# Performance work log

Hardware: AMD Instinct MI355X
Metric: run time of the kernel (lower is better)

Reference implementation:

```python
import jax, jax.numpy as jnp
import numpy as np

B, T, C = 2, 2048, 2048
NH, NKV = 32, 8
HD = C // NH          # 64
G = NH // NKV         # queries per kv head

def setup_inputs() -> dict:
    key = jax.random.key(0)
    ks = jax.random.split(key, 6)
    s = 0.02
    return {
        "x":  jax.random.normal(ks[0], (B, T, C), jnp.float32),
        "wq": jax.random.normal(ks[1], (C, C), jnp.float32) * s,
        "wk": jax.random.normal(ks[2], (C, NKV * HD), jnp.float32) * s,
        "wv": jax.random.normal(ks[3], (C, NKV * HD), jnp.float32) * s,
        "wp": jax.random.normal(ks[4], (C, C), jnp.float32) * s,
        "bp": jax.random.normal(ks[5], (C,), jnp.float32) * s,
    }

def reference(x, wq, wk, wv, wp, bp):
    Bb, Tt, Cc = x.shape
    # projections
    q = (x @ wq).reshape(Bb, Tt, NH, HD).transpose(0, 2, 1, 3)    # (B, NH, T, D)
    k = (x @ wk).reshape(Bb, Tt, NKV, HD).transpose(0, 2, 1, 3)   # (B, NKV, T, D)
    v = (x @ wv).reshape(Bb, Tt, NKV, HD).transpose(0, 2, 1, 3)
    # GQA: group query heads per kv head (equivalent to repeat_interleave on kv)
    qg = q.reshape(Bb, NKV, G, Tt, HD)                            # (B, NKV, G, T, D)
    att = jnp.einsum('bhgqd,bhkd->bhgqk', qg, k) * (HD ** -0.5)   # (B, NKV, G, T, T)
    causal = jnp.tril(jnp.ones((Tt, Tt), bool))
    att = jnp.where(causal, att, -jnp.inf)
    att = jax.nn.softmax(att, axis=-1)
    y = jnp.einsum('bhgqk,bhkd->bhgqd', att, v)                   # (B, NKV, G, T, D)
    y = y.reshape(Bb, NH, Tt, HD).transpose(0, 2, 1, 3).reshape(Bb, Tt, Cc)
    return y @ wp + bp
```

## Files before the change

kernel.cpp:

```cpp
#include <hip/hip_runtime.h>
#include <math.h>

#define B_   2
#define T_   2048
#define C_   2048
#define NH_  32
#define NKV_ 8
#define HD_  64
#define G_   (NH_ / NKV_)
#define M_   (B_ * T_)
#define C3_  3072

typedef __attribute__((ext_vector_type(8))) short  short8;
typedef __attribute__((ext_vector_type(4))) float  f32x4;

__device__ __forceinline__ short f2bf(float f) {
    unsigned u = __float_as_uint(f);
    unsigned r = (u + 0x7FFFu + ((u >> 16) & 1u)) >> 16;
    return (short)r;
}

__device__ __forceinline__ void gload_lds16(const void* g, void* l) {
    __builtin_amdgcn_global_load_lds(
        (const __attribute__((address_space(1))) unsigned int*)g,
        (__attribute__((address_space(3))) unsigned int*)l, 16, 0, 0);
}

__global__ __launch_bounds__(256)
void cast_f32_bf16(const float* __restrict__ in, short* __restrict__ out, int n8)
{
    int i = blockIdx.x * blockDim.x + threadIdx.x;
    const int stride = gridDim.x * blockDim.x;
    for (; i < n8; i += stride) {
        const float4 a = ((const float4*)in)[i * 2];
        const float4 b = ((const float4*)in)[i * 2 + 1];
        short8 v;
        v[0] = f2bf(a.x); v[1] = f2bf(a.y); v[2] = f2bf(a.z); v[3] = f2bf(a.w);
        v[4] = f2bf(b.x); v[5] = f2bf(b.y); v[6] = f2bf(b.z); v[7] = f2bf(b.w);
        ((short8*)out)[i] = v;
    }
}

__global__ __launch_bounds__(256)
void transpose_cast(const float* __restrict__ W, short* __restrict__ Wt,
                    int Nw, int rowOff)
{
    __shared__ float tileF[64][65];
    const int tid = threadIdx.x;
    const int n0 = blockIdx.x * 64;
    const int k0 = blockIdx.y * 64;

    #pragma unroll
    for (int it = 0; it < 4; ++it) {
        const int s = it * 256 + tid;
        const int r = s >> 4;
        const int c4 = (s & 15) * 4;
        const float4 v = *(const float4*)(W + (size_t)(k0 + r) * Nw + n0 + c4);
        tileF[r][c4 + 0] = v.x;
        tileF[r][c4 + 1] = v.y;
        tileF[r][c4 + 2] = v.z;
        tileF[r][c4 + 3] = v.w;
    }
    __syncthreads();
    #pragma unroll
    for (int it = 0; it < 2; ++it) {
        const int s = it * 256 + tid;
        const int n = s >> 3;
        const int kc = (s & 7) * 8;
        short8 v;
        #pragma unroll
        for (int j = 0; j < 8; ++j) v[j] = f2bf(tileF[kc + j][n]);
        *(short8*)&Wt[(size_t)(rowOff + n0 + n) * 2048 + k0 + kc] = v;
    }
}

__global__ __launch_bounds__(256)
void transpose_v_bf16(const short* __restrict__ QKVb, short* __restrict__ Vt)
{
    __shared__ short Ls[64 * 66];
    const int tid = threadIdx.x;
    const int t0  = blockIdx.x * 64;
    const int b   = blockIdx.y >> 3;
    const int kvh = blockIdx.y & 7;

    #pragma unroll
    for (int it = 0; it < 2; ++it) {
        const int s = it * 256 + tid;
        const int tr = s >> 3;
        const int c8 = (s & 7) * 8;
        const short8 v = *(const short8*)(
            QKVb + (size_t)(b * T_ + t0 + tr) * C3_ + 2560 + kvh * HD_ + c8);
        #pragma unroll
        for (int e = 0; e < 8; ++e) Ls[tr * 66 + c8 + e] = v[e];
    }
    __syncthreads();
    #pragma unroll
    for (int it = 0; it < 2; ++it) {
        const int s = it * 256 + tid;
        const int d  = s >> 3;
        const int t8 = (s & 7) * 8;
        short8 v;
        #pragma unroll
        for (int j = 0; j < 8; ++j) v[j] = Ls[(t8 + j) * 66 + d];
        *(short8*)(Vt + (size_t)(blockIdx.y * HD_ + d) * T_ + t0 + t8) = v;
    }
}

__global__ __launch_bounds__(256)
void gemm_bf16_bt(const short* __restrict__ A, const short* __restrict__ Bt,
                  float* __restrict__ C, short* __restrict__ Cb,
                  const float* __restrict__ bias, int M, int N, int K)
{
    __shared__ __attribute__((aligned(16))) short Als[128 * 32];
    __shared__ __attribute__((aligned(16))) short Bls[128 * 32];

    const int tid  = threadIdx.x;
    const int wave = tid >> 6;
    const int lane = tid & 63;

    const int gx   = gridDim.x;
    const int nwg  = gx * gridDim.y;
    const int orig = blockIdx.y * gx + blockIdx.x;
    const int qc   = nwg >> 3;
    const int rc   = nwg & 7;
    const int xcd  = orig & 7;
    const int wgid = (xcd < rc ? xcd * (qc + 1) : rc * (qc + 1) + (xcd - rc) * qc)
                     + (orig >> 3);
    const int m0 = (wgid / gx) * 128;
    const int n0 = (wgid % gx) * 128;

    const int wr = wave >> 1;
    const int wc = wave & 1;

    const int sr = lane >> 2;
    const int kq = (lane & 3) * 8;
    const int fr = lane & 15;
    const int fg = (lane >> 4) * 8;

    const short* Abase = A  + (size_t)m0 * K;
    const short* Bbase = Bt + (size_t)n0 * K;

    f32x4 acc[4][4];
    const f32x4 zero = {0.f, 0.f, 0.f, 0.f};
    #pragma unroll
    for (int i = 0; i < 4; ++i)
        #pragma unroll
        for (int j = 0; j < 4; ++j) acc[i][j] = zero;

    for (int k0 = 0; k0 < K; k0 += 32) {
        __syncthreads();
        #pragma unroll
        for (int i = 0; i < 2; ++i) {
            const int c = wave * 2 + i;
            const int row = c * 16 + sr;
            gload_lds16(Abase + (size_t)row * K + k0 + kq, &Als[c * 512]);
            gload_lds16(Bbase + (size_t)row * K + k0 + kq, &Bls[c * 512]);
        }
        __syncthreads();

        short8 af[4], bf[4];
        #pragma unroll
        for (int mi = 0; mi < 4; ++mi)
            af[mi] = *(const short8*)&Als[(wr * 64 + mi * 16 + fr) * 32 + fg];
        #pragma unroll
        for (int ni = 0; ni < 4; ++ni)
            bf[ni] = *(const short8*)&Bls[(wc * 64 + ni * 16 + fr) * 32 + fg];
        #pragma unroll
        for (int mi = 0; mi < 4; ++mi)
            #pragma unroll
            for (int ni = 0; ni < 4; ++ni)
                acc[mi][ni] = __builtin_amdgcn_mfma_f32_16x16x32_bf16(
                    af[mi], bf[ni], acc[mi][ni], 0, 0, 0);
    }

    const int rsub = (lane >> 4) * 4;
    const int ccol0 = n0 + wc * 64 + fr;
    #pragma unroll
    for (int mi = 0; mi < 4; ++mi) {
        const int mrow = m0 + wr * 64 + mi * 16 + rsub;
        #pragma unroll
        for (int ni = 0; ni < 4; ++ni) {
            const int col = ccol0 + ni * 16;
            const float badd = bias ? bias[col] : 0.f;
            #pragma unroll
            for (int r = 0; r < 4; ++r) {
                const float v = acc[mi][ni][r] + badd;
                if (Cb) Cb[(size_t)(mrow + r) * N + col] = f2bf(v);
                else    C [(size_t)(mrow + r) * N + col] = v;
            }
        }
    }
}

__global__ __launch_bounds__(256)
void attn_mfma(const short* __restrict__ QKVb, const short* __restrict__ Vt,
               short* __restrict__ Yb)
{
    __shared__ __attribute__((aligned(16))) short Kls[2][4096];
    __shared__ __attribute__((aligned(16))) short Vls[2][4096];
    __shared__ __attribute__((aligned(16))) short Pls[4096];

    const int tid  = threadIdx.x;
    const int wave = tid >> 6;
    const int lane = tid & 63;
    const int bh = blockIdx.y;
    const int b   = bh >> 5;
    const int h   = bh & 31;
    const int kvh = h >> 2;
    const int bx  = gridDim.x - 1 - blockIdx.x;
    const int m0 = bx * 64;
    const int qbase = m0 + wave * 16;

    const int fr = lane & 15;
    const int fg = (lane >> 4) * 8;
    const int g4 = (lane >> 4) * 4;

    const short* qrow = QKVb + (size_t)(b * T_ + qbase + fr) * C3_ + h * HD_;
    const short8 qa0 = *(const short8*)(qrow + fg);
    const short8 qa1 = *(const short8*)(qrow + 32 + fg);

    f32x4 accO[4];
    const f32x4 zero = {0.f, 0.f, 0.f, 0.f};
    #pragma unroll
    for (int i = 0; i < 4; ++i) accO[i] = zero;
    float lsum[4] = {0.f, 0.f, 0.f, 0.f};

    const int sr  = lane >> 3;
    const int scb = (lane & 7) * 16;
    const int ssw = (scb ^ ((sr & 7) << 4)) >> 1;
    const short* Kg = QKVb + (size_t)b * T_ * C3_ + 2048 + kvh * HD_ + ssw;
    const short* Vg = Vt + (size_t)(b * NKV_ + kvh) * HD_ * T_ + ssw;

    short* PlsW = Pls + wave * 1024;
    const char* PlsB = (const char*)PlsW;

    const int ntiles = bx + 1;
    const int frsw = (fr & 7) << 4;

    auto STAGE = [&](int t, int bsel) {
        const int ks = t * 64;
        #pragma unroll
        for (int i = 0; i < 2; ++i) {
            const int c = wave * 2 + i;
            gload_lds16(Kg + (size_t)(ks + c * 8 + sr) * C3_, &Kls[bsel][c * 512]);
            gload_lds16(Vg + (size_t)(c * 8 + sr) * T_ + ks,  &Vls[bsel][c * 512]);
        }
    };

    STAGE(0, 0);
    __syncthreads();

    int cur = 0;
    for (int t = 0; t < ntiles; ++t) {
        if (t + 1 < ntiles) STAGE(t + 1, cur ^ 1);

        const int ks = t * 64;
        const char* KlsB = (const char*)&Kls[cur][0];
        const char* VlsB = (const char*)&Vls[cur][0];

        f32x4 accS[4];
        #pragma unroll
        for (int jt = 0; jt < 4; ++jt) accS[jt] = zero;
        __builtin_amdgcn_s_setprio(1);
        #pragma unroll
        for (int jt = 0; jt < 4; ++jt) {
            const int row = jt * 16 + fr;
            const char* base = KlsB + row * 128;
            const short8 kb0 = *(const short8*)(base + ((fg * 2) ^ frsw));
            const short8 kb1 = *(const short8*)(base + (((32 + fg) * 2) ^ frsw));
            accS[jt] = __builtin_amdgcn_mfma_f32_16x16x32_bf16(qa0, kb0, accS[jt], 0, 0, 0);
            accS[jt] = __builtin_amdgcn_mfma_f32_16x16x32_bf16(qa1, kb1, accS[jt], 0, 0, 0);
        }
        __builtin_amdgcn_s_setprio(0);

        const bool full = (ks + 63 <= qbase);
        float pv[4][4];
        #pragma unroll
        for (int jt = 0; jt < 4; ++jt) {
            #pragma unroll
            for (int r = 0; r < 4; ++r) {
                const int j = ks + jt * 16 + fr;
                const int q = qbase + g4 + r;
                float p = __expf(fmaf(accS[jt][r], 0.125f, -4.0f));
                if (!full && j > q) p = 0.f;
                pv[jt][r] = p;
            }
        }
        #pragma unroll
        for (int r = 0; r < 4; ++r)
            lsum[r] += (pv[0][r] + pv[1][r]) + (pv[2][r] + pv[3][r]);

        #pragma unroll
        for (int jt = 0; jt < 4; ++jt) {
            #pragma unroll
            for (int r = 0; r < 4; ++r) {
                const int prow = g4 + r;
                const int pj = jt * 16 + fr;
                *(short*)((char*)PlsW + prow * 128 + ((pj * 2) ^ ((prow & 7) << 4)))
                    = f2bf(pv[jt][r]);
            }
        }

        __builtin_amdgcn_s_setprio(1);
        #pragma unroll
        for (int kk = 0; kk < 2; ++kk) {
            const int kcb = (kk * 32 + fg) * 2;
            const short8 pa = *(const short8*)(PlsB + fr * 128 + (kcb ^ frsw));
            #pragma unroll
            for (int ni = 0; ni < 4; ++ni) {
                const int row = ni * 16 + fr;
                const short8 vb = *(const short8*)(VlsB + row * 128 + (kcb ^ frsw));
                accO[ni] = __builtin_amdgcn_mfma_f32_16x16x32_bf16(pa, vb, accO[ni], 0, 0, 0);
            }
        }
        __builtin_amdgcn_s_setprio(0);

        if (t + 1 < ntiles) { __syncthreads(); cur ^= 1; }
    }

    #pragma unroll
    for (int r = 0; r < 4; ++r) {
        float v = lsum[r];
        v += __shfl_xor(v, 1);
        v += __shfl_xor(v, 2);
        v += __shfl_xor(v, 4);
        v += __shfl_xor(v, 8);
        lsum[r] = 1.f / v;
    }

    #pragma unroll
    for (int ni = 0; ni < 4; ++ni)
        #pragma unroll
        for (int r = 0; r < 4; ++r)
            PlsW[(g4 + r) * 64 + ni * 16 + fr] = f2bf(accO[ni][r] * lsum[r]);

    #pragma unroll
    for (int i = 0; i < 2; ++i) {
        const int lin = i * 1024 + lane * 16;
        const int rr = lin >> 7;
        const int cb = lin & 127;
        const short8 v = *(const short8*)(PlsB + lin);
        *(short8*)((char*)Yb + ((size_t)(b * T_ + qbase + rr) * C_ + h * HD_) * 2 + cb) = v;
    }
}

extern "C" void kernel_launch(void* const* d_in, const int* in_sizes, int n_in,
                              void* d_out, int out_size, void* d_ws, size_t ws_size,
                              hipStream_t stream)
{
    const float* x  = (const float*)d_in[0];
    const float* wq = (const float*)d_in[1];
    const float* wk = (const float*)d_in[2];
    const float* wv = (const float*)d_in[3];
    const float* wp = (const float*)d_in[4];
    const float* bp = (const float*)d_in[5];
    float* out = (float*)d_out;

    char* w = (char*)d_ws;
    short* xb   = (short*)w;
    short* wt   = (short*)(w + 16777216);
    short* QKVb = (short*)(w + 29360128);
    short* Vt   = (short*)(w + 54525952);
    short* Yb   = xb;
    short* wpt  = wt;

    const dim3 blk(256);

    cast_f32_bf16<<<2048, blk, 0, stream>>>(x, xb, M_ * C_ / 8);

    transpose_cast<<<dim3(32, 32), blk, 0, stream>>>(wq, wt, 2048, 0);
    transpose_cast<<<dim3(8, 32),  blk, 0, stream>>>(wk, wt, 512, 2048);
    transpose_cast<<<dim3(8, 32),  blk, 0, stream>>>(wv, wt, 512, 2560);

    gemm_bf16_bt<<<dim3(C3_ / 128, M_ / 128), blk, 0, stream>>>(
        xb, wt, nullptr, QKVb, nullptr, M_, C3_, C_);

    transpose_cast<<<dim3(32, 32), blk, 0, stream>>>(wp, wpt, 2048, 0);
    transpose_v_bf16<<<dim3(32, 16), blk, 0, stream>>>(QKVb, Vt);

    attn_mfma<<<dim3(T_ / 64, B_ * NH_), blk, 0, stream>>>(QKVb, Vt, Yb);

    gemm_bf16_bt<<<dim3(C_ / 128, M_ / 128), blk, 0, stream>>>(
        Yb, wpt, out, nullptr, bp, M_, C_, C_);
}
```

Measured before the change: 377.0 us.

## Process 128 query rows per attention block, two 16-row groups per wave

The attention kernel now gives each block 128 query rows, and each wave handles two 16-row groups that share the K/V tiles staged in LDS. Each staged K/V tile is reused across twice as many queries, which halves global and LDS staging traffic per query and the number of barriers per unit of work. Waves whose rows lie entirely before a tile skip its compute. The cost is higher register pressure, half as many blocks in the grid, and intra-block causal imbalance.

```diff
diff --git a/kernel.cpp b/kernel.cpp
--- a/kernel.cpp
+++ b/kernel.cpp
@@ -208,22 +208,27 @@
     const int h   = bh & 31;
     const int kvh = h >> 2;
     const int bx  = gridDim.x - 1 - blockIdx.x;
-    const int m0 = bx * 64;
-    const int qbase = m0 + wave * 16;
+    const int m0 = bx * 128;
+    const int qbase = m0 + wave * 32;
 
     const int fr = lane & 15;
     const int fg = (lane >> 4) * 8;
     const int g4 = (lane >> 4) * 4;
 
-    const short* qrow = QKVb + (size_t)(b * T_ + qbase + fr) * C3_ + h * HD_;
-    const short8 qa0 = *(const short8*)(qrow + fg);
-    const short8 qa1 = *(const short8*)(qrow + 32 + fg);
-
-    f32x4 accO[4];
+    const short* qrow0 = QKVb + (size_t)(b * T_ + qbase + fr) * C3_ + h * HD_;
+    const short* qrow1 = qrow0 + 16 * C3_;
+    const short8 qa00 = *(const short8*)(qrow0 + fg);
+    const short8 qa01 = *(const short8*)(qrow0 + 32 + fg);
+    const short8 qa10 = *(const short8*)(qrow1 + fg);
+    const short8 qa11 = *(const short8*)(qrow1 + 32 + fg);
+
+    f32x4 accO[2][4];
     const f32x4 zero = {0.f, 0.f, 0.f, 0.f};
     #pragma unroll
-    for (int i = 0; i < 4; ++i) accO[i] = zero;
-    float lsum[4] = {0.f, 0.f, 0.f, 0.f};
+    for (int rg = 0; rg < 2; ++rg)
+        #pragma unroll
+        for (int i = 0; i < 4; ++i) accO[rg][i] = zero;
+    float lsum[2][4] = {{0.f,0.f,0.f,0.f},{0.f,0.f,0.f,0.f}};
 
     const int sr  = lane >> 3;
     const int scb = (lane & 7) * 16;
@@ -234,7 +239,7 @@
     short* PlsW = Pls + wave * 1024;
     const char* PlsB = (const char*)PlsW;
 
-    const int ntiles = bx + 1;
+    const int ntiles = 2 * bx + 2;
     const int frsw = (fr & 7) << 4;
 
     auto STAGE = [&](int t, int bsel) {
@@ -258,89 +263,106 @@
         const char* KlsB = (const char*)&Kls[cur][0];
         const char* VlsB = (const char*)&Vls[cur][0];
 
-        f32x4 accS[4];
-        #pragma unroll
-        for (int jt = 0; jt < 4; ++jt) accS[jt] = zero;
-        __builtin_amdgcn_s_setprio(1);
-        #pragma unroll
-        for (int jt = 0; jt < 4; ++jt) {
-            const int row = jt * 16 + fr;
-            const char* base = KlsB + row * 128;
-            const short8 kb0 = *(const short8*)(base + ((fg * 2) ^ frsw));
-            const short8 kb1 = *(const short8*)(base + (((32 + fg) * 2) ^ frsw));
-            accS[jt] = __builtin_amdgcn_mfma_f32_16x16x32_bf16(qa0, kb0, accS[jt], 0, 0, 0);
-            accS[jt] = __builtin_amdgcn_mfma_f32_16x16x32_bf16(qa1, kb1, accS[jt], 0, 0, 0);
-        }
-        __builtin_amdgcn_s_setprio(0);
-
-        const bool full = (ks + 63 <= qbase);
-        float pv[4][4];
-        #pragma unroll
-        for (int jt = 0; jt < 4; ++jt) {
-            #pragma unroll
-            for (int r = 0; r < 4; ++r) {
-                const int j = ks + jt * 16 + fr;
-                const int q = qbase + g4 + r;
-                float p = __expf(fmaf(accS[jt][r], 0.125f, -4.0f));
-                if (!full && j > q) p = 0.f;
-                pv[jt][r] = p;
+        if (ks <= qbase + 31) {
+            f32x4 accS[2][4];
+            #pragma unroll
+            for (int rg = 0; rg < 2; ++rg)
+                #pragma unroll
+                for (int jt = 0; jt < 4; ++jt) accS[rg][jt] = zero;
+            __builtin_amdgcn_s_setprio(1);
+            #pragma unroll
+            for (int jt = 0; jt < 4; ++jt) {
+                const int row = jt * 16 + fr;
+                const char* base = KlsB + row * 128;
+                const short8 kb0 = *(const short8*)(base + ((fg * 2) ^ frsw));
+                const short8 kb1 = *(const short8*)(base + (((32 + fg) * 2) ^ frsw));
+                accS[0][jt] = __builtin_amdgcn_mfma_f32_16x16x32_bf16(qa00, kb0, accS[0][jt], 0, 0, 0);
+                accS[0][jt] = __builtin_amdgcn_mfma_f32_16x16x32_bf16(qa01, kb1, accS[0][jt], 0, 0, 0);
+                accS[1][jt] = __builtin_amdgcn_mfma_f32_16x16x32_bf16(qa10, kb0, accS[1][jt], 0, 0, 0);
+                accS[1][jt] = __builtin_amdgcn_mfma_f32_16x16x32_bf16(qa11, kb1, accS[1][jt], 0, 0, 0);
             }
-        }
-        #pragma unroll
-        for (int r = 0; r < 4; ++r)
-            lsum[r] += (pv[0][r] + pv[1][r]) + (pv[2][r] + pv[3][r]);
-
-        #pragma unroll
-        for (int jt = 0; jt < 4; ++jt) {
-            #pragma unroll
-            for (int r = 0; r < 4; ++r) {
-                const int prow = g4 + r;
-                const int pj = jt * 16 + fr;
-                *(short*)((char*)PlsW + prow * 128 + ((pj * 2) ^ ((prow & 7) << 4)))
-                    = f2bf(pv[jt][r]);
+            __builtin_amdgcn_s_setprio(0);
+
+            #pragma unroll
+            for (int rg = 0; rg < 2; ++rg) {
+                const int qb = qbase + rg * 16;
+                const bool full = (ks + 63 <= qb);
+
+                float pv[4][4];
+                #pragma unroll
+                for (int jt = 0; jt < 4; ++jt) {
+                    #pragma unroll
+                    for (int r = 0; r < 4; ++r) {
+                        const int j = ks + jt * 16 + fr;
+                        const int q = qb + g4 + r;
+                        float p = __expf(fmaf(accS[rg][jt][r], 0.125f, -4.0f));
+                        if (!full && j > q) p = 0.f;
+                        pv[jt][r] = p;
+                    }
+                }
+                #pragma unroll
+                for (int r = 0; r < 4; ++r)
+                    lsum[rg][r] += (pv[0][r] + pv[1][r]) + (pv[2][r] + pv[3][r]);
+
+                #pragma unroll
+                for (int jt = 0; jt < 4; ++jt) {
+                    #pragma unroll
+                    for (int r = 0; r < 4; ++r) {
+                        const int prow = g4 + r;
+                        const int pj = jt * 16 + fr;
+                        *(short*)((char*)PlsW + prow * 128 + ((pj * 2) ^ ((prow & 7) << 4)))
+                            = f2bf(pv[jt][r]);
+                    }
+                }
+
+                __builtin_amdgcn_s_setprio(1);
+                #pragma unroll
+                for (int kk = 0; kk < 2; ++kk) {
+                    const int kcb = (kk * 32 + fg) * 2;
+                    const short8 pa = *(const short8*)(PlsB + fr * 128 + (kcb ^ frsw));
+                    #pragma unroll
+                    for (int ni = 0; ni < 4; ++ni) {
+                        const int row = ni * 16 + fr;
+                        const short8 vb = *(const short8*)(VlsB + row * 128 + (kcb ^ frsw));
+                        accO[rg][ni] = __builtin_amdgcn_mfma_f32_16x16x32_bf16(pa, vb, accO[rg][ni], 0, 0, 0);
+                    }
+                }
+                __builtin_amdgcn_s_setprio(0);
             }
         }
 
-        __builtin_amdgcn_s_setprio(1);
-        #pragma unroll
-        for (int kk = 0; kk < 2; ++kk) {
-            const int kcb = (kk * 32 + fg) * 2;
-            const short8 pa = *(const short8*)(PlsB + fr * 128 + (kcb ^ frsw));
-            #pragma unroll
-            for (int ni = 0; ni < 4; ++ni) {
-                const int row = ni * 16 + fr;
-                const short8 vb = *(const short8*)(VlsB + row * 128 + (kcb ^ frsw));
-                accO[ni] = __builtin_amdgcn_mfma_f32_16x16x32_bf16(pa, vb, accO[ni], 0, 0, 0);
-            }
-        }
-        __builtin_amdgcn_s_setprio(0);
-
         if (t + 1 < ntiles) { __syncthreads(); cur ^= 1; }
     }
 
     #pragma unroll
-    for (int r = 0; r < 4; ++r) {
-        float v = lsum[r];
-        v += __shfl_xor(v, 1);
-        v += __shfl_xor(v, 2);
-        v += __shfl_xor(v, 4);
-        v += __shfl_xor(v, 8);
-        lsum[r] = 1.f / v;
-    }
-
-    #pragma unroll
-    for (int ni = 0; ni < 4; ++ni)
-        #pragma unroll
-        for (int r = 0; r < 4; ++r)
-            PlsW[(g4 + r) * 64 + ni * 16 + fr] = f2bf(accO[ni][r] * lsum[r]);
-
-    #pragma unroll
-    for (int i = 0; i < 2; ++i) {
-        const int lin = i * 1024 + lane * 16;
-        const int rr = lin >> 7;
-        const int cb = lin & 127;
-        const short8 v = *(const short8*)(PlsB + lin);
-        *(short8*)((char*)Yb + ((size_t)(b * T_ + qbase + rr) * C_ + h * HD_) * 2 + cb) = v;
+    for (int rg = 0; rg < 2; ++rg)
+        #pragma unroll
+        for (int r = 0; r < 4; ++r) {
+            float v = lsum[rg][r];
+            v += __shfl_xor(v, 1);
+            v += __shfl_xor(v, 2);
+            v += __shfl_xor(v, 4);
+            v += __shfl_xor(v, 8);
+            lsum[rg][r] = 1.f / v;
+        }
+
+    #pragma unroll
+    for (int rg = 0; rg < 2; ++rg) {
+        #pragma unroll
+        for (int ni = 0; ni < 4; ++ni)
+            #pragma unroll
+            for (int r = 0; r < 4; ++r)
+                PlsW[(g4 + r) * 64 + ni * 16 + fr] = f2bf(accO[rg][ni][r] * lsum[rg][r]);
+
+        #pragma unroll
+        for (int i = 0; i < 2; ++i) {
+            const int lin = i * 1024 + lane * 16;
+            const int rr = lin >> 7;
+            const int cb = lin & 127;
+            const short8 v = *(const short8*)(PlsB + lin);
+            *(short8*)((char*)Yb +
+                ((size_t)(b * T_ + qbase + rg * 16 + rr) * C_ + h * HD_) * 2 + cb) = v;
+        }
     }
 }
 
@@ -378,7 +400,7 @@
     transpose_cast<<<dim3(32, 32), blk, 0, stream>>>(wp, wpt, 2048, 0);
     transpose_v_bf16<<<dim3(32, 16), blk, 0, stream>>>(QKVb, Vt);
 
-    attn_mfma<<<dim3(T_ / 64, B_ * NH_), blk, 0, stream>>>(QKVb, Vt, Yb);
+    attn_mfma<<<dim3(T_ / 128, B_ * NH_), blk, 0, stream>>>(QKVb, Vt, Yb);
 
     gemm_bf16_bt<<<dim3(C_ / 128, M_ / 128), blk, 0, stream>>>(
         Yb, wpt, out, nullptr, bp, M_, C_, C_);
```

Measured after the change: 383.0 us. No clear change (+1.6%).
